# Optimization experiments

Measured on AMD Instinct MI355X. Metric: run time of the kernel, lower is better.

Reference implementation:

```python
import jax, jax.numpy as jnp
import numpy as np

VOCAB, S, D, H, DH, L, W1S, DFF = 50265, 4096, 768, 12, 64, 2, 256, 3072


def layer_norm(x, g, b, eps=1e-5):
    m = jnp.mean(x, axis=-1, keepdims=True)
    v = jnp.mean((x - m) ** 2, axis=-1, keepdims=True)
    return (x - m) * jax.lax.rsqrt(v + eps) * g + b


def sliding_global_attn(q, k, v, att, w=W1S):
    # q,k,v: [B,H,S,Dh]; att: [B,S] float (1 real / 0 pad). Longformer-style
    # sliding window (one-sided w) + global attention on token 0.
    B, nh, S_, Dh = q.shape
    nc = S_ // w
    q = q * (Dh ** -0.5)
    k_pad = jnp.pad(k, ((0, 0), (0, 0), (w, w), (0, 0)))
    v_pad = jnp.pad(v, ((0, 0), (0, 0), (w, w), (0, 0)))
    idx = jnp.arange(nc)[:, None] * w + jnp.arange(3 * w)[None, :]  # [nc,3w] into padded axis
    k_band = k_pad[:, :, idx]  # [B,H,nc,3w,Dh]
    v_band = v_pad[:, :, idx]
    qc = q.reshape(B, nh, nc, w, Dh)
    s_loc = jnp.einsum('bhcqd,bhckd->bhcqk', qc, k_band)  # [B,H,nc,w,3w]
    rel = jnp.arange(3 * w)[None, :] - jnp.arange(w)[:, None]  # [w,3w]
    band_ok = (rel >= 0) & (rel <= 2 * w)
    key_abs = idx - w  # [nc,3w] absolute key positions
    in_seq = (key_abs >= 0) & (key_abs < S_) & (key_abs != 0)  # token 0 handled by global column
    key_real = att[:, jnp.clip(key_abs, 0, S_ - 1)] > 0  # [B,nc,3w]
    valid = band_ok[None, None, None] & in_seq[None, None, :, None, :] & key_real[:, None, :, None, :]
    s_loc = jnp.where(valid, s_loc, -1e9)
    s_g = jnp.einsum('bhcqd,bhd->bhcq', qc, k[:, :, 0])  # global key column
    p = jax.nn.softmax(jnp.concatenate([s_g[..., None], s_loc], axis=-1), axis=-1)
    out = (jnp.einsum('bhcq,bhd->bhcqd', p[..., 0], v[:, :, 0])
           + jnp.einsum('bhcqk,bhckd->bhcqd', p[..., 1:], v_band)).reshape(B, nh, S_, Dh)
    # global token 0 attends to everything
    s0 = jnp.where(att[:, None, :] > 0, jnp.einsum('bhd,bhsd->bhs', q[:, :, 0], k), -1e9)
    out0 = jnp.einsum('bhs,bhsd->bhd', jax.nn.softmax(s0, axis=-1), v)
    return out.at[:, :, 0].set(out0)


def setup_inputs() -> dict:
    key = jax.random.key(0)
    ks = jax.random.split(key, 16)
    sc = 0.02
    inp = {
        'input_ids': jax.random.randint(ks[0], (2, S), 0, VOCAB, dtype=jnp.int64)
        if jax.config.jax_enable_x64 else jax.random.randint(ks[0], (2, S), 0, VOCAB, dtype=jnp.int32),
        'attention_mask': jnp.ones((2, S), dtype=jnp.int32),
        'word_emb': sc * jax.random.normal(ks[1], (VOCAB, D), jnp.float32),
        'pos_emb': sc * jax.random.normal(ks[2], (S, D), jnp.float32),
        'emb_ln_g': jnp.ones((D,), jnp.float32), 'emb_ln_b': jnp.zeros((D,), jnp.float32),
        'Wq': sc * jax.random.normal(ks[3], (L, D, D), jnp.float32), 'bq': jnp.zeros((L, D), jnp.float32),
        'Wk': sc * jax.random.normal(ks[4], (L, D, D), jnp.float32), 'bk': jnp.zeros((L, D), jnp.float32),
        'Wv': sc * jax.random.normal(ks[5], (L, D, D), jnp.float32), 'bv': jnp.zeros((L, D), jnp.float32),
        'Wo': sc * jax.random.normal(ks[6], (L, D, D), jnp.float32), 'bo': jnp.zeros((L, D), jnp.float32),
        'ln1_g': jnp.ones((L, D), jnp.float32), 'ln1_b': jnp.zeros((L, D), jnp.float32),
        'Wf1': sc * jax.random.normal(ks[7], (L, D, DFF), jnp.float32), 'bf1': jnp.zeros((L, DFF), jnp.float32),
        'Wf2': sc * jax.random.normal(ks[8], (L, DFF, D), jnp.float32), 'bf2': jnp.zeros((L, D), jnp.float32),
        'ln2_g': jnp.ones((L, D), jnp.float32), 'ln2_b': jnp.zeros((L, D), jnp.float32),
        'Wh1': sc * jax.random.normal(ks[9], (D, 256), jnp.float32), 'bh1': jnp.zeros((256,), jnp.float32),
        'Wh2': sc * jax.random.normal(ks[10], (256, 14), jnp.float32), 'bh2': jnp.zeros((14,), jnp.float32),
    }
    return inp


def reference(input_ids, attention_mask, word_emb, pos_emb, emb_ln_g, emb_ln_b,
              Wq, bq, Wk, bk, Wv, bv, Wo, bo, ln1_g, ln1_b,
              Wf1, bf1, Wf2, bf2, ln2_g, ln2_b, Wh1, bh1, Wh2, bh2):
    B, S_ = input_ids.shape
    att = attention_mask.astype(jnp.float32)
    x = word_emb[input_ids] + pos_emb[None, :S_, :]
    x = layer_norm(x, emb_ln_g, emb_ln_b)
    for l in range(L):
        def heads(w, b):
            return (x @ w + b).reshape(B, S_, H, DH).transpose(0, 2, 1, 3)
        q = heads(Wq[l], bq[l]); k = heads(Wk[l], bk[l]); v = heads(Wv[l], bv[l])
        a = sliding_global_attn(q, k, v, att)
        a = a.transpose(0, 2, 1, 3).reshape(B, S_, D) @ Wo[l] + bo[l]
        x = layer_norm(x + a, ln1_g[l], ln1_b[l])
        f = jax.nn.gelu(x @ Wf1[l] + bf1[l]) @ Wf2[l] + bf2[l]
        x = layer_norm(x + f, ln2_g[l], ln2_b[l])
    # masked mean pool
    m = att[..., None]
    pooled = jnp.sum(x * m, axis=1) / jnp.clip(jnp.sum(m, axis=1), 1e-9)
    h = jax.nn.relu(pooled @ Wh1 + bh1)
    return jax.nn.sigmoid(h @ Wh2 + bh2) * 4.0
```

## Files before the change

kernel.cpp:

```cpp
#include <hip/hip_runtime.h>
#include <hip/hip_bf16.h>
#include <math.h>

#define S_LEN 4096
#define D_MODEL 768
#define NHEAD 12
#define DH 64
#define NLAYER 2
#define DFF 3072
#define BATCH 2
#define QSTR 2304

typedef __attribute__((ext_vector_type(8))) __bf16 bf16x8;
typedef __attribute__((ext_vector_type(4))) float f32x4;
typedef __attribute__((ext_vector_type(16))) float f32x16;

__device__ __forceinline__ unsigned short f2bf_bits(float f) {
  unsigned int u = __float_as_uint(f);
  unsigned int r = (u + 0x7fffu + ((u >> 16) & 1u)) >> 16;
  return (unsigned short)r;
}

__device__ __forceinline__ float bf2f(unsigned short u) {
  return __uint_as_float(((unsigned int)u) << 16);
}

__device__ __forceinline__ unsigned int cvtpk_bf16(float lo, float hi) {
  unsigned int d;
  asm("v_cvt_pk_bf16_f32 %0, %1, %2" : "=v"(d) : "v"(lo), "v"(hi));
  return d;
}

__device__ __forceinline__ float gelu_fast(float x) {
  float u = 0.7978845608028654f * (x + 0.044715f * x * x * x);
  float t2 = fminf(fmaxf(2.f * u, -18.f), 18.f);
  float e = __expf(t2);
  return 0.5f * x * (1.f + (e - 1.f) / (e + 1.f));
}

#define ASYNC_COPY16(gsrc, ldst)                                       \
  __builtin_amdgcn_global_load_lds(                                    \
      (const __attribute__((address_space(1))) void*)(gsrc),           \
      (__attribute__((address_space(3))) void*)(ldst), 16, 0, 0)

#define MFMA_BF16(a, b, c) __builtin_amdgcn_mfma_f32_16x16x32_bf16(a, b, c, 0, 0, 0)
#define MFMA32_BF16(a, b, c) __builtin_amdgcn_mfma_f32_32x32x16_bf16(a, b, c, 0, 0, 0)

__device__ __forceinline__ float blk_sum256(float v, float* lds) {
#pragma unroll
  for (int off = 32; off > 0; off >>= 1) v += __shfl_down(v, off, 64);
  __syncthreads();
  if ((threadIdx.x & 63) == 0) lds[threadIdx.x >> 6] = v;
  __syncthreads();
  return lds[0] + lds[1] + lds[2] + lds[3];
}

__global__ __launch_bounds__(256) void wconv_kernel(
    const float* __restrict__ Wq, const float* __restrict__ Wk,
    const float* __restrict__ Wv, const float* __restrict__ Wo,
    const float* __restrict__ Wf1, const float* __restrict__ Wf2,
    unsigned short* __restrict__ Wbf) {
  int id = blockIdx.x;
  const float* src;
  unsigned short* dst;
  int K, N, t;
  if (id < 4608) {
    int m = id / 576;
    t = id % 576;
    int layer = m >> 2, which = m & 3;
    const float* s = (which == 0) ? Wq : (which == 1) ? Wk : (which == 2) ? Wv : Wo;
    src = s + (size_t)layer * 589824;
    dst = Wbf + (size_t)layer * 7077888 + (size_t)which * 589824;
    K = 768; N = 768;
  } else if (id < 9216) {
    int j = id - 4608;
    int layer = j / 2304;
    t = j % 2304;
    src = Wf1 + (size_t)layer * 2359296;
    dst = Wbf + (size_t)layer * 7077888 + 2359296;
    K = 768; N = 3072;
  } else {
    int j = id - 9216;
    int layer = j / 2304;
    t = j % 2304;
    src = Wf2 + (size_t)layer * 2359296;
    dst = Wbf + (size_t)layer * 7077888 + 4718592;
    K = 3072; N = 768;
  }
  int tiles_n = N >> 5;
  int tk = t / tiles_n, tn = t % tiles_n;
  __shared__ float tile[32][33];
  int c = threadIdx.x & 31, r0 = threadIdx.x >> 5;
#pragma unroll
  for (int p = 0; p < 4; ++p) {
    int r = r0 + p * 8;
    tile[r][c] = src[(size_t)(tk * 32 + r) * N + tn * 32 + c];
  }
  __syncthreads();
#pragma unroll
  for (int p = 0; p < 4; ++p) {
    int r = r0 + p * 8;
    dst[(size_t)(tn * 32 + r) * K + tk * 32 + c] = f2bf_bits(tile[c][r]);
  }
}

__global__ __launch_bounds__(256) void mask_kernel(
    const int* __restrict__ att, float* __restrict__ maskF) {
  int i = blockIdx.x * 256 + threadIdx.x;
  int b = i >> 12, ka = i & 4095;
  maskF[i] = (ka >= 1 && att[b * S_LEN + ka] > 0) ? 0.f : -1e9f;
}

__global__ __launch_bounds__(256) void embed_ln_kernel(
    const int* __restrict__ ids, const float* __restrict__ wemb,
    const float* __restrict__ pemb, const float* __restrict__ g,
    const float* __restrict__ b, unsigned short* __restrict__ Xb) {
  int row = blockIdx.x;
  int s = row % S_LEN;
  int id = ids[row];
  const float* we = wemb + (size_t)id * D_MODEL;
  const float* pe = pemb + (size_t)s * D_MODEL;
  int t = threadIdx.x;
  __shared__ float lds[4];
  float v0 = we[t] + pe[t];
  float v1 = we[t + 256] + pe[t + 256];
  float v2 = we[t + 512] + pe[t + 512];
  float mean = blk_sum256(v0 + v1 + v2, lds) * (1.f / 768.f);
  float d0 = v0 - mean, d1 = v1 - mean, d2 = v2 - mean;
  float var = blk_sum256(d0 * d0 + d1 * d1 + d2 * d2, lds) * (1.f / 768.f);
  float rs = rsqrtf(var + 1e-5f);
  unsigned short* xb = Xb + (size_t)row * D_MODEL;
  xb[t]       = f2bf_bits(d0 * rs * g[t] + b[t]);
  xb[t + 256] = f2bf_bits(d1 * rs * g[t + 256] + b[t + 256]);
  xb[t + 512] = f2bf_bits(d2 * rs * g[t + 512] + b[t + 512]);
}

__global__ __launch_bounds__(256) void ln_kernel(
    const float* __restrict__ T, const float* __restrict__ g,
    const float* __restrict__ b, unsigned short* __restrict__ Xb) {
  int row = blockIdx.x;
  const float* tp = T + (size_t)row * D_MODEL;
  int t = threadIdx.x;
  __shared__ float lds[4];
  float v0 = tp[t], v1 = tp[t + 256], v2 = tp[t + 512];
  float mean = blk_sum256(v0 + v1 + v2, lds) * (1.f / 768.f);
  float d0 = v0 - mean, d1 = v1 - mean, d2 = v2 - mean;
  float var = blk_sum256(d0 * d0 + d1 * d1 + d2 * d2, lds) * (1.f / 768.f);
  float rs = rsqrtf(var + 1e-5f);
  unsigned short* xb = Xb + (size_t)row * D_MODEL;
  xb[t]       = f2bf_bits(d0 * rs * g[t] + b[t]);
  xb[t + 256] = f2bf_bits(d1 * rs * g[t + 256] + b[t + 256]);
  xb[t + 512] = f2bf_bits(d2 * rs * g[t + 512] + b[t + 512]);
}

template <int MODE>
__global__ __launch_bounds__(256) void gemm32(
    const unsigned short* __restrict__ A, const unsigned short* __restrict__ Bt,
    const float* __restrict__ bias0, const float* __restrict__ bias1,
    const float* __restrict__ bias2, const unsigned short* __restrict__ ResBf,
    void* __restrict__ Cout, int M, int N, int K) {
  __shared__ unsigned short Abuf[3][128 * 32];
  __shared__ unsigned short Bbuf[3][128 * 32];
  const int tid = threadIdx.x;
  const int lane = tid & 63, w = tid >> 6;
  const int wm = w >> 1, wn = w & 1;
  const int l31 = lane & 31, l5 = lane >> 5;

  const int nbx = gridDim.x;
  const int nwg = nbx * gridDim.y;
  const int orig = blockIdx.y * nbx + blockIdx.x;
  const int wgid = (orig & 7) * (nwg >> 3) + (orig >> 3);
  const int m0 = (wgid / nbx) * 128, n0 = (wgid % nbx) * 128;

  f32x16 acc[2][2];
#pragma unroll
  for (int i = 0; i < 2; ++i)
#pragma unroll
    for (int j = 0; j < 2; ++j)
#pragma unroll
      for (int r = 0; r < 16; ++r) acc[i][j][r] = 0.f;

  const int s0 = w * 64 + lane, s1 = s0 + 256;
  const int r0 = s0 >> 2, c0 = (s0 & 3) ^ ((r0 >> 1) & 3);
  const int r1 = s1 >> 2, c1 = (s1 & 3) ^ ((r1 >> 1) & 3);
  const unsigned short* gA0 = A + (size_t)(m0 + r0) * K + c0 * 8;
  const unsigned short* gA1 = A + (size_t)(m0 + r1) * K + c1 * 8;
  const unsigned short* gB0 = Bt + (size_t)(n0 + r0) * K + c0 * 8;
  const unsigned short* gB1 = Bt + (size_t)(n0 + r1) * K + c1 * 8;
  const int dA0 = (w * 64) * 8, dA1 = (256 + w * 64) * 8;

  int aoff[2][2], boff[2][2];
#pragma unroll
  for (int mt = 0; mt < 2; ++mt) {
    int ra = wm * 64 + mt * 32 + l31;
    int rb = wn * 64 + mt * 32 + l31;
    int key_a = (ra >> 1) & 3, key_b = (rb >> 1) & 3;
#pragma unroll
    for (int ks = 0; ks < 2; ++ks) {
      aoff[mt][ks] = ra * 32 + ((((ks << 1) | l5) ^ key_a) << 3);
      boff[mt][ks] = rb * 32 + ((((ks << 1) | l5) ^ key_b) << 3);
    }
  }

#define STAGE(bsel)                                                       \
  {                                                                       \
    ASYNC_COPY16(gA0, &Abuf[bsel][dA0]);                                  \
    ASYNC_COPY16(gA1, &Abuf[bsel][dA1]);                                  \
    ASYNC_COPY16(gB0, &Bbuf[bsel][dA0]);                                  \
    ASYNC_COPY16(gB1, &Bbuf[bsel][dA1]);                                  \
    gA0 += 32; gA1 += 32; gB0 += 32; gB1 += 32;                           \
  }

  const int nk = K >> 5;
  STAGE(0);
  if (nk > 1) STAGE(1);
  asm volatile("s_waitcnt vmcnt(4)" ::: "memory");
  __builtin_amdgcn_s_barrier();
  __builtin_amdgcn_sched_barrier(0);

  int cur = 0;
  for (int kt = 0; kt < nk; ++kt) {
    if (kt + 2 < nk) {
      int nxt = cur + 2;
      if (nxt >= 3) nxt -= 3;
      STAGE(nxt);
    }
    bf16x8 av[2][2], bv[2][2];
#pragma unroll
    for (int mt = 0; mt < 2; ++mt)
#pragma unroll
      for (int ks = 0; ks < 2; ++ks) {
        av[mt][ks] = *(const bf16x8*)(&Abuf[cur][aoff[mt][ks]]);
        bv[mt][ks] = *(const bf16x8*)(&Bbuf[cur][boff[mt][ks]]);
      }
#pragma unroll
    for (int mt = 0; mt < 2; ++mt)
#pragma unroll
      for (int nt = 0; nt < 2; ++nt)
#pragma unroll
        for (int ks = 0; ks < 2; ++ks)
          acc[mt][nt] = MFMA32_BF16(av[mt][ks], bv[nt][ks], acc[mt][nt]);
    if (kt + 1 < nk) {
      if (kt + 2 < nk)
        asm volatile("s_waitcnt vmcnt(4)" ::: "memory");
      else
        asm volatile("s_waitcnt vmcnt(0)" ::: "memory");
      __builtin_amdgcn_s_barrier();
      __builtin_amdgcn_sched_barrier(0);
    }
    cur = (cur == 2) ? 0 : cur + 1;
  }
#undef STAGE

#pragma unroll
  for (int mt = 0; mt < 2; ++mt) {
#pragma unroll
    for (int nt = 0; nt < 2; ++nt) {
      int gc = n0 + wn * 64 + nt * 32 + l31;
      float bsv;
      if (MODE == 4)
        bsv = (gc < 768) ? bias0[gc] : (gc < 1536) ? bias1[gc - 768] : bias2[gc - 1536];
      else
        bsv = bias0[gc];
#pragma unroll
      for (int reg = 0; reg < 16; ++reg) {
        int gr = m0 + wm * 64 + mt * 32 + (reg & 3) + 8 * (reg >> 2) + 4 * l5;
        float v = acc[mt][nt][reg] + bsv;
        if (MODE == 1) v = gelu_fast(v);
        if (MODE == 4 && gc < 768) v *= 0.125f;
        if (MODE == 2) {
          v += bf2f(ResBf[(size_t)gr * 768 + gc]);
          ((float*)Cout)[(size_t)gr * N + gc] = v;
        } else {
          ((unsigned short*)Cout)[(size_t)gr * N + gc] = f2bf_bits(v);
        }
      }
    }
  }
}

__global__ __launch_bounds__(256) void vtrans_kernel(
    const unsigned short* __restrict__ Vsrc, unsigned short* __restrict__ Vt) {
  int kb = blockIdx.x, h = blockIdx.y, b = blockIdx.z;
  int k0 = kb * 64;
  const size_t bs = (size_t)b * S_LEN;
  const size_t bh = (size_t)(b * NHEAD + h);
  __shared__ unsigned short tile[64][72];
  int tid = threadIdx.x;
#pragma unroll
  for (int p = 0; p < 2; ++p) {
    int idx = p * 256 + tid;
    int key = idx >> 3, ch = idx & 7;
    bf16x8 v = *(const bf16x8*)(Vsrc + (bs + k0 + key) * QSTR + h * DH + ch * 8);
    *(bf16x8*)&tile[key][ch * 8] = v;
  }
  __syncthreads();
#pragma unroll
  for (int p = 0; p < 2; ++p) {
    int idx = p * 256 + tid;
    int d = idx >> 3, kc = idx & 7;
    unsigned int w0 = tile[kc * 8 + 0][d] | ((unsigned int)tile[kc * 8 + 1][d] << 16);
    unsigned int w1 = tile[kc * 8 + 2][d] | ((unsigned int)tile[kc * 8 + 3][d] << 16);
    unsigned int w2 = tile[kc * 8 + 4][d] | ((unsigned int)tile[kc * 8 + 5][d] << 16);
    unsigned int w3 = tile[kc * 8 + 6][d] | ((unsigned int)tile[kc * 8 + 7][d] << 16);
    uint4 out = make_uint4(w0, w1, w2, w3);
    *(uint4*)(Vt + (bh * 64 + d) * S_LEN + k0 + kc * 8) = out;
  }
}

__global__ __launch_bounds__(512) void band_attn_kernel(
    const unsigned short* __restrict__ Qg, const unsigned short* __restrict__ Kgb,
    const unsigned short* __restrict__ Vgb, const unsigned short* __restrict__ Vt,
    const int* __restrict__ att, const float* __restrict__ maskF,
    unsigned short* __restrict__ Aout) {
  const int bid = blockIdx.x;
  const int tid = threadIdx.x;
  const int lane = tid & 63, wq = tid >> 6;
  const int g = lane >> 4, cl = lane & 15;

  __shared__ __align__(16) float smemg[4680];

  if (bid >= 384) {
    int g2 = bid - 384;
    int h = g2 % NHEAD, b = g2 / NHEAD;
    const size_t bs = (size_t)b * S_LEN;
    float* sc = smemg;
    float* q0 = sc + S_LEN;
    float* red = q0 + 64;
    float* part = red + 8;
    if (tid < 64) q0[tid] = bf2f(Qg[bs * QSTR + h * DH + tid]);
    __syncthreads();
    float lmax = -1e30f;
    for (int s = tid; s < S_LEN; s += 512) {
      const unsigned short* kp = Kgb + (bs + s) * QSTR + h * DH;
      float acc = 0.f;
#pragma unroll
      for (int cc = 0; cc < 8; ++cc) {
        uint4 u = *(const uint4*)(kp + cc * 8);
        const unsigned int* uu = (const unsigned int*)&u;
#pragma unroll
        for (int w2 = 0; w2 < 4; ++w2) {
          unsigned int x = uu[w2];
          acc += q0[cc * 8 + w2 * 2] * __uint_as_float(x << 16);
          acc += q0[cc * 8 + w2 * 2 + 1] * __uint_as_float(x & 0xffff0000u);
        }
      }
      acc = (att[b * S_LEN + s] > 0) ? acc : -1e9f;
      sc[s] = acc;
      lmax = fmaxf(lmax, acc);
    }
#pragma unroll
    for (int off = 32; off > 0; off >>= 1) lmax = fmaxf(lmax, __shfl_down(lmax, off, 64));
    __syncthreads();
    if (lane == 0) red[wq] = lmax;
    __syncthreads();
    float M = red[0];
#pragma unroll
    for (int i = 1; i < 8; ++i) M = fmaxf(M, red[i]);
    float lsum = 0.f;
    for (int s = tid; s < S_LEN; s += 512) {
      float p = __expf(sc[s] - M);
      sc[s] = p;
      lsum += p;
    }
#pragma unroll
    for (int off = 32; off > 0; off >>= 1) lsum += __shfl_down(lsum, off, 64);
    __syncthreads();
    if (lane == 0) red[wq] = lsum;
    __syncthreads();
    float L = red[0];
#pragma unroll
    for (int i = 1; i < 8; ++i) L += red[i];
    int d = tid & 63, chunk = tid >> 6;
    float acc2 = 0.f;
    for (int s = chunk * 512; s < (chunk + 1) * 512; ++s)
      acc2 += sc[s] * bf2f(Vgb[(bs + s) * QSTR + h * DH + d]);
    part[chunk * 64 + d] = acc2;
    __syncthreads();
    if (tid < 64) {
      float v = 0.f;
#pragma unroll
      for (int i = 0; i < 8; ++i) v += part[i * 64 + tid];
      Aout[bs * D_MODEL + h * DH + tid] = f2bf_bits(v / L);
    }
    return;
  }

  const int xcd = bid & 7, within = bid >> 3;
  const int flat = xcd * 48 + within;
  const int c = flat & 15;
  const int hb = flat >> 4;
  const int h = hb % NHEAD, b = hb / NHEAD;
  const size_t bs = (size_t)b * S_LEN;
  const size_t bh = (size_t)(b * NHEAD + h);
  const int Q0 = c * 256;

  bf16x8 qf[2][2];
#pragma unroll
  for (int qt = 0; qt < 2; ++qt)
#pragma unroll
    for (int ks = 0; ks < 2; ++ks)
      qf[qt][ks] = *(const bf16x8*)(Qg + (bs + Q0 + wq * 32 + qt * 16 + cl) * QSTR +
                                    h * DH + ks * 32 + g * 8);

  float mrun[2], lrun[2];
  f32x4 oacc[2][4];
#pragma unroll
  for (int qt = 0; qt < 2; ++qt) {
    float sg = 0.f;
#pragma unroll
    for (int ks = 0; ks < 2; ++ks) {
      bf16x8 k0 = *(const bf16x8*)(Kgb + bs * QSTR + h * DH + ks * 32 + g * 8);
#pragma unroll
      for (int j = 0; j < 8; ++j) sg += (float)qf[qt][ks][j] * (float)k0[j];
    }
    sg += __shfl_xor(sg, 16, 64);
    sg += __shfl_xor(sg, 32, 64);
    mrun[qt] = sg;
    lrun[qt] = 1.f;
  }
#pragma unroll
  for (int dt = 0; dt < 4; ++dt) {
    float v0d = bf2f(Vgb[bs * QSTR + h * DH + dt * 16 + cl]);
    f32x4 vv = {v0d, v0d, v0d, v0d};
    oacc[0][dt] = vv;
    oacc[1][dt] = vv;
  }

  const int jlo = wq * 32, jhi = wq * 32 + 543;
  const int tlo = (Q0 < 256) ? 4 : 0;
  int thi = (S_LEN + 256 - Q0) >> 6;
  if (thi > 12) thi = 12;

  for (int t = tlo; t < thi; ++t) {
    if (t * 64 + 63 < jlo || t * 64 > jhi) continue;
    const int kabs0 = Q0 - 256 + t * 64;

    f32x4 accs[4][2];
#pragma unroll
    for (int kt = 0; kt < 4; ++kt) {
      accs[kt][0] = (f32x4){0.f, 0.f, 0.f, 0.f};
      accs[kt][1] = (f32x4){0.f, 0.f, 0.f, 0.f};
    }
#pragma unroll
    for (int ks = 0; ks < 2; ++ks) {
      bf16x8 kf[4];
#pragma unroll
      for (int kt = 0; kt < 4; ++kt)
        kf[kt] = *(const bf16x8*)(Kgb + (bs + kabs0 + kt * 16 + cl) * QSTR +
                                  h * DH + ks * 32 + g * 8);
#pragma unroll
      for (int kt = 0; kt < 4; ++kt) {
        accs[kt][0] = MFMA_BF16(kf[kt], qf[0][ks], accs[kt][0]);
        accs[kt][1] = MFMA_BF16(kf[kt], qf[1][ks], accs[kt][1]);
      }
    }

    float4 mk[4];
#pragma unroll
    for (int kt = 0; kt < 4; ++kt)
      mk[kt] = *(const float4*)(maskF + b * S_LEN + kabs0 + kt * 16 + g * 4);

#pragma unroll
    for (int qt = 0; qt < 2; ++qt) {
      int iq = wq * 32 + qt * 16 + cl;
      int relbase = t * 64 - iq;
      float pvv[4][4];
      float tmax = -1e30f;
#pragma unroll
      for (int kt = 0; kt < 4; ++kt) {
        const float* mkf = (const float*)&mk[kt];
#pragma unroll
        for (int r = 0; r < 4; ++r) {
          int key = kt * 16 + g * 4 + r;
          int rel = relbase + key;
          float x = accs[kt][qt][r] + mkf[r];
          x = (rel >= 0 && rel <= 512) ? x : -1e9f;
          pvv[kt][r] = x;
          tmax = fmaxf(tmax, x);
        }
      }
      tmax = fmaxf(tmax, __shfl_xor(tmax, 16, 64));
      tmax = fmaxf(tmax, __shfl_xor(tmax, 32, 64));
      float mnew = fmaxf(mrun[qt], tmax);
      float scale = __expf(mrun[qt] - mnew);
      mrun[qt] = mnew;
      float psum = 0.f;
#pragma unroll
      for (int kt = 0; kt < 4; ++kt)
#pragma unroll
        for (int r = 0; r < 4; ++r) {
          float pp = __expf(pvv[kt][r] - mnew);
          pvv[kt][r] = pp;
          psum += pp;
        }
      psum += __shfl_xor(psum, 16, 64);
      psum += __shfl_xor(psum, 32, 64);
      lrun[qt] = lrun[qt] * scale + psum;
      float scr[4];
#pragma unroll
      for (int r = 0; r < 4; ++r) scr[r] = __shfl(scale, g * 4 + r, 64);
#pragma unroll
      for (int dt = 0; dt < 4; ++dt) {
        oacc[qt][dt][0] *= scr[0];
        oacc[qt][dt][1] *= scr[1];
        oacc[qt][dt][2] *= scr[2];
        oacc[qt][dt][3] *= scr[3];
      }
#pragma unroll
      for (int ks = 0; ks < 2; ++ks) {
        unsigned int E0D0 = cvtpk_bf16(pvv[ks * 2][0], pvv[ks * 2][1]);
        unsigned int E0D1 = cvtpk_bf16(pvv[ks * 2][2], pvv[ks * 2][3]);
        unsigned int E1D0 = cvtpk_bf16(pvv[ks * 2 + 1][0], pvv[ks * 2 + 1][1]);
        unsigned int E1D1 = cvtpk_bf16(pvv[ks * 2 + 1][2], pvv[ks * 2 + 1][3]);
        int src0 = ((lane >> 4) & 1) * 32 + cl;
        int src1 = src0 + 16;
        unsigned int a0 = (unsigned int)__shfl((int)E0D0, src0, 64);
        unsigned int a1 = (unsigned int)__shfl((int)E0D1, src0, 64);
        unsigned int a2 = (unsigned int)__shfl((int)E0D0, src1, 64);
        unsigned int a3 = (unsigned int)__shfl((int)E0D1, src1, 64);
        unsigned int b0 = (unsigned int)__shfl((int)E1D0, src0, 64);
        unsigned int b1 = (unsigned int)__shfl((int)E1D1, src0, 64);
        unsigned int b2 = (unsigned int)__shfl((int)E1D0, src1, 64);
        unsigned int b3 = (unsigned int)__shfl((int)E1D1, src1, 64);
        bool hi = lane >= 32;
        union { unsigned int u[4]; bf16x8 v; } af;
        af.u[0] = hi ? b0 : a0;
        af.u[1] = hi ? b1 : a1;
        af.u[2] = hi ? b2 : a2;
        af.u[3] = hi ? b3 : a3;
#pragma unroll
        for (int dt = 0; dt < 4; ++dt) {
          bf16x8 vf = *(const bf16x8*)(Vt + (bh * 64 + dt * 16 + cl) * S_LEN +
                                       kabs0 + (ks * 4 + g) * 8);
          oacc[qt][dt] = MFMA_BF16(af.v, vf, oacc[qt][dt]);
        }
      }
    }
  }

#pragma unroll
  for (int qt = 0; qt < 2; ++qt) {
    float lr[4];
#pragma unroll
    for (int r = 0; r < 4; ++r) lr[r] = 1.f / __shfl(lrun[qt], g * 4 + r, 64);
#pragma unroll
    for (int dt = 0; dt < 4; ++dt)
#pragma unroll
      for (int r = 0; r < 4; ++r) {
        int row = Q0 + wq * 32 + qt * 16 + g * 4 + r;
        if (row != 0)
          Aout[(bs + row) * D_MODEL + h * DH + dt * 16 + cl] =
              f2bf_bits(oacc[qt][dt][r] * lr[r]);
      }
  }
}

__global__ __launch_bounds__(256) void pool1_kernel(
    const unsigned short* __restrict__ Xb, const int* __restrict__ att,
    float* __restrict__ ppart) {
  int sb = blockIdx.x, b = blockIdx.y, t = threadIdx.x;
  float a0 = 0.f, a1 = 0.f, a2 = 0.f;
  for (int s = sb * 256; s < sb * 256 + 256; ++s) {
    float a = (float)att[b * S_LEN + s];
    const unsigned short* xp = Xb + ((size_t)b * S_LEN + s) * D_MODEL;
    a0 += bf2f(xp[t]) * a; a1 += bf2f(xp[t + 256]) * a; a2 += bf2f(xp[t + 512]) * a;
  }
  float* pp = ppart + ((size_t)b * 16 + sb) * D_MODEL;
  pp[t] = a0; pp[t + 256] = a1; pp[t + 512] = a2;
}

__global__ __launch_bounds__(256) void pool2_kernel(
    const float* __restrict__ ppart, const int* __restrict__ att,
    float* __restrict__ pooled) {
  int b = blockIdx.x, t = threadIdx.x;
  float a0 = 0.f, a1 = 0.f, a2 = 0.f;
  for (int sb = 0; sb < 16; ++sb) {
    const float* pp = ppart + ((size_t)b * 16 + sb) * D_MODEL;
    a0 += pp[t]; a1 += pp[t + 256]; a2 += pp[t + 512];
  }
  float cnt = 0.f;
  for (int s = 0; s < S_LEN; ++s) cnt += (float)att[b * S_LEN + s];
  cnt = fmaxf(cnt, 1e-9f);
  pooled[b * D_MODEL + t]       = a0 / cnt;
  pooled[b * D_MODEL + t + 256] = a1 / cnt;
  pooled[b * D_MODEL + t + 512] = a2 / cnt;
}

__global__ __launch_bounds__(256) void head_kernel(
    const float* __restrict__ pooled, const float* __restrict__ Wh1,
    const float* __restrict__ bh1, const float* __restrict__ Wh2,
    const float* __restrict__ bh2, float* __restrict__ out) {
  __shared__ float hbuf[2][256];
  int t = threadIdx.x;
  for (int b = 0; b < 2; ++b) {
    float acc = bh1[t];
    for (int d = 0; d < D_MODEL; ++d) acc += pooled[b * D_MODEL + d] * Wh1[d * 256 + t];
    hbuf[b][t] = fmaxf(acc, 0.f);
  }
  __syncthreads();
  if (t < 28) {
    int b = t / 14, j = t % 14;
    float acc = bh2[j];
    for (int i = 0; i < 256; ++i) acc += hbuf[b][i] * Wh2[i * 14 + j];
    out[t] = 4.f / (1.f + __expf(-acc));
  }
}

extern "C" void kernel_launch(void* const* d_in, const int* in_sizes, int n_in,
                              void* d_out, int out_size, void* d_ws,
                              size_t ws_size, hipStream_t stream) {
  const int* ids    = (const int*)d_in[0];
  const int* att    = (const int*)d_in[1];
  const float* wemb = (const float*)d_in[2];
  const float* pemb = (const float*)d_in[3];
  const float* elng = (const float*)d_in[4];
  const float* elnb = (const float*)d_in[5];
  const float* Wq   = (const float*)d_in[6];
  const float* bq   = (const float*)d_in[7];
  const float* Wk   = (const float*)d_in[8];
  const float* bk   = (const float*)d_in[9];
  const float* Wv   = (const float*)d_in[10];
  const float* bv   = (const float*)d_in[11];
  const float* Wo   = (const float*)d_in[12];
  const float* bo   = (const float*)d_in[13];
  const float* ln1g = (const float*)d_in[14];
  const float* ln1b = (const float*)d_in[15];
  const float* Wf1  = (const float*)d_in[16];
  const float* bf1  = (const float*)d_in[17];
  const float* Wf2  = (const float*)d_in[18];
  const float* bf2  = (const float*)d_in[19];
  const float* ln2g = (const float*)d_in[20];
  const float* ln2b = (const float*)d_in[21];
  const float* Wh1  = (const float*)d_in[22];
  const float* bh1  = (const float*)d_in[23];
  const float* Wh2  = (const float*)d_in[24];
  const float* bh2  = (const float*)d_in[25];

  const int M = BATCH * S_LEN;
  float* ws = (float*)d_ws;
  float* T = ws;
  unsigned short* QKV  = (unsigned short*)(ws + 6291456);
  unsigned short* Vt   = (unsigned short*)(ws + 11010048);
  unsigned short* Abbf = (unsigned short*)(ws + 12582912);
  unsigned short* Xbf  = (unsigned short*)(ws + 15728640);
  unsigned short* FFbf = (unsigned short*)(ws + 18874368);
  unsigned short* Wbf  = (unsigned short*)(ws + 31457280);
  float* pooled = ws + 38535168;
  float* ppart  = ws + 38536704;
  float* maskF  = ws + 38561280;

  wconv_kernel<<<13824, 256, 0, stream>>>(Wq, Wk, Wv, Wo, Wf1, Wf2, Wbf);
  mask_kernel<<<32, 256, 0, stream>>>(att, maskF);
  embed_ln_kernel<<<M, 256, 0, stream>>>(ids, wemb, pemb, elng, elnb, Xbf);

  for (int l = 0; l < NLAYER; ++l) {
    const unsigned short* wqkv = Wbf + (size_t)l * 7077888;
    const unsigned short* wot  = wqkv + 1769472;
    const unsigned short* wf1t = wqkv + 2359296;
    const unsigned short* wf2t = wqkv + 4718592;

    gemm32<4><<<dim3(18, 64), 256, 0, stream>>>(
        Xbf, wqkv, bq + l * D_MODEL, bk + l * D_MODEL, bv + l * D_MODEL,
        nullptr, QKV, M, QSTR, 768);

    vtrans_kernel<<<dim3(64, NHEAD, BATCH), 256, 0, stream>>>(QKV + 1536, Vt);
    band_attn_kernel<<<408, 512, 0, stream>>>(
        QKV, QKV + 768, QKV + 1536, Vt, att, maskF, Abbf);

    gemm32<2><<<dim3(6, 64), 256, 0, stream>>>(
        Abbf, wot, bo + l * D_MODEL, nullptr, nullptr, Xbf, T, M, 768, 768);
    ln_kernel<<<M, 256, 0, stream>>>(T, ln1g + l * D_MODEL, ln1b + l * D_MODEL, Xbf);

    gemm32<1><<<dim3(24, 64), 256, 0, stream>>>(
        Xbf, wf1t, bf1 + l * DFF, nullptr, nullptr, nullptr, FFbf, M, DFF, 768);
    gemm32<2><<<dim3(6, 64), 256, 0, stream>>>(
        FFbf, wf2t, bf2 + l * D_MODEL, nullptr, nullptr, Xbf, T, M, 768, DFF);
    ln_kernel<<<M, 256, 0, stream>>>(T, ln2g + l * D_MODEL, ln2b + l * D_MODEL, Xbf);
  }

  pool1_kernel<<<dim3(16, BATCH), 256, 0, stream>>>(Xbf, att, ppart);
  pool2_kernel<<<BATCH, 256, 0, stream>>>(ppart, att, pooled);
  head_kernel<<<1, 256, 0, stream>>>(pooled, Wh1, bh1, Wh2, bh2, (float*)d_out);
}
```

Before: 851.1 us.

## Rewrite band attention with 32x32 MFMA, per-wave key range, smaller blocks

The band attention kernel moves from 16x16x16 MFMA tiles with two query subtiles per wave to 32x32 MFMA tiles, where each lane owns one query row and the softmax reductions need only a single cross-half shuffle. Each wave now loops only over the key tiles its own 32 queries touch, replacing the fixed 12-tile loop that skipped tiles with a branch. Blocks shrink to 256 threads and 128 queries, doubling the grid, and the global-token path is adjusted to four waves. The aim is fewer shuffles, less wasted tile work and better occupancy and load balance. The P-operand lane shuffling for the second MFMA is new and error-prone.

```diff
diff --git a/kernel.cpp b/kernel.cpp
--- a/kernel.cpp
+++ b/kernel.cpp
@@ -308,7 +308,7 @@
   }
 }
 
-__global__ __launch_bounds__(512) void band_attn_kernel(
+__global__ __launch_bounds__(256) void band_attn_kernel(
     const unsigned short* __restrict__ Qg, const unsigned short* __restrict__ Kgb,
     const unsigned short* __restrict__ Vgb, const unsigned short* __restrict__ Vt,
     const int* __restrict__ att, const float* __restrict__ maskF,
@@ -316,12 +316,12 @@
   const int bid = blockIdx.x;
   const int tid = threadIdx.x;
   const int lane = tid & 63, wq = tid >> 6;
-  const int g = lane >> 4, cl = lane & 15;
-
-  __shared__ __align__(16) float smemg[4680];
-
-  if (bid >= 384) {
-    int g2 = bid - 384;
+  const int l31 = lane & 31, l5 = lane >> 5;
+
+  __shared__ __align__(16) float smemg[4424];
+
+  if (bid >= 768) {
+    int g2 = bid - 768;
     int h = g2 % NHEAD, b = g2 / NHEAD;
     const size_t bs = (size_t)b * S_LEN;
     float* sc = smemg;
@@ -331,7 +331,7 @@
     if (tid < 64) q0[tid] = bf2f(Qg[bs * QSTR + h * DH + tid]);
     __syncthreads();
     float lmax = -1e30f;
-    for (int s = tid; s < S_LEN; s += 512) {
+    for (int s = tid; s < S_LEN; s += 256) {
       const unsigned short* kp = Kgb + (bs + s) * QSTR + h * DH;
       float acc = 0.f;
 #pragma unroll
@@ -354,11 +354,9 @@
     __syncthreads();
     if (lane == 0) red[wq] = lmax;
     __syncthreads();
-    float M = red[0];
-#pragma unroll
-    for (int i = 1; i < 8; ++i) M = fmaxf(M, red[i]);
+    float M = fmaxf(fmaxf(red[0], red[1]), fmaxf(red[2], red[3]));
     float lsum = 0.f;
-    for (int s = tid; s < S_LEN; s += 512) {
+    for (int s = tid; s < S_LEN; s += 256) {
       float p = __expf(sc[s] - M);
       sc[s] = p;
       lsum += p;
@@ -368,190 +366,161 @@
     __syncthreads();
     if (lane == 0) red[wq] = lsum;
     __syncthreads();
-    float L = red[0];
-#pragma unroll
-    for (int i = 1; i < 8; ++i) L += red[i];
+    float L = red[0] + red[1] + red[2] + red[3];
     int d = tid & 63, chunk = tid >> 6;
     float acc2 = 0.f;
-    for (int s = chunk * 512; s < (chunk + 1) * 512; ++s)
+    for (int s = chunk * 1024; s < (chunk + 1) * 1024; ++s)
       acc2 += sc[s] * bf2f(Vgb[(bs + s) * QSTR + h * DH + d]);
     part[chunk * 64 + d] = acc2;
     __syncthreads();
     if (tid < 64) {
-      float v = 0.f;
-#pragma unroll
-      for (int i = 0; i < 8; ++i) v += part[i * 64 + tid];
+      float v = part[tid] + part[64 + tid] + part[128 + tid] + part[192 + tid];
       Aout[bs * D_MODEL + h * DH + tid] = f2bf_bits(v / L);
     }
     return;
   }
 
   const int xcd = bid & 7, within = bid >> 3;
-  const int flat = xcd * 48 + within;
-  const int c = flat & 15;
-  const int hb = flat >> 4;
+  const int flat = xcd * 96 + within;
+  const int c = flat & 31;
+  const int hb = flat >> 5;
   const int h = hb % NHEAD, b = hb / NHEAD;
   const size_t bs = (size_t)b * S_LEN;
   const size_t bh = (size_t)(b * NHEAD + h);
-  const int Q0 = c * 256;
-
-  bf16x8 qf[2][2];
-#pragma unroll
-  for (int qt = 0; qt < 2; ++qt)
-#pragma unroll
-    for (int ks = 0; ks < 2; ++ks)
-      qf[qt][ks] = *(const bf16x8*)(Qg + (bs + Q0 + wq * 32 + qt * 16 + cl) * QSTR +
-                                    h * DH + ks * 32 + g * 8);
-
-  float mrun[2], lrun[2];
-  f32x4 oacc[2][4];
-#pragma unroll
-  for (int qt = 0; qt < 2; ++qt) {
+  const int qbase = c * 128 + wq * 32;
+  const int iq = qbase + l31;
+
+  bf16x8 qfr[4];
+#pragma unroll
+  for (int ks = 0; ks < 4; ++ks)
+    qfr[ks] = *(const bf16x8*)(Qg + (bs + iq) * QSTR + h * DH + ks * 16 + l5 * 8);
+
+  float mrun, lrun;
+  {
     float sg = 0.f;
 #pragma unroll
-    for (int ks = 0; ks < 2; ++ks) {
-      bf16x8 k0 = *(const bf16x8*)(Kgb + bs * QSTR + h * DH + ks * 32 + g * 8);
-#pragma unroll
-      for (int j = 0; j < 8; ++j) sg += (float)qf[qt][ks][j] * (float)k0[j];
-    }
-    sg += __shfl_xor(sg, 16, 64);
+    for (int ks = 0; ks < 4; ++ks) {
+      bf16x8 k0 = *(const bf16x8*)(Kgb + bs * QSTR + h * DH + ks * 16 + l5 * 8);
+#pragma unroll
+      for (int j = 0; j < 8; ++j) sg += (float)qfr[ks][j] * (float)k0[j];
+    }
     sg += __shfl_xor(sg, 32, 64);
-    mrun[qt] = sg;
-    lrun[qt] = 1.f;
-  }
-#pragma unroll
-  for (int dt = 0; dt < 4; ++dt) {
-    float v0d = bf2f(Vgb[bs * QSTR + h * DH + dt * 16 + cl]);
-    f32x4 vv = {v0d, v0d, v0d, v0d};
-    oacc[0][dt] = vv;
-    oacc[1][dt] = vv;
-  }
-
-  const int jlo = wq * 32, jhi = wq * 32 + 543;
-  const int tlo = (Q0 < 256) ? 4 : 0;
-  int thi = (S_LEN + 256 - Q0) >> 6;
-  if (thi > 12) thi = 12;
-
-  for (int t = tlo; t < thi; ++t) {
-    if (t * 64 + 63 < jlo || t * 64 > jhi) continue;
-    const int kabs0 = Q0 - 256 + t * 64;
-
-    f32x4 accs[4][2];
-#pragma unroll
-    for (int kt = 0; kt < 4; ++kt) {
-      accs[kt][0] = (f32x4){0.f, 0.f, 0.f, 0.f};
-      accs[kt][1] = (f32x4){0.f, 0.f, 0.f, 0.f};
-    }
-#pragma unroll
-    for (int ks = 0; ks < 2; ++ks) {
-      bf16x8 kf[4];
-#pragma unroll
-      for (int kt = 0; kt < 4; ++kt)
-        kf[kt] = *(const bf16x8*)(Kgb + (bs + kabs0 + kt * 16 + cl) * QSTR +
-                                  h * DH + ks * 32 + g * 8);
-#pragma unroll
-      for (int kt = 0; kt < 4; ++kt) {
-        accs[kt][0] = MFMA_BF16(kf[kt], qf[0][ks], accs[kt][0]);
-        accs[kt][1] = MFMA_BF16(kf[kt], qf[1][ks], accs[kt][1]);
-      }
-    }
-
-    float4 mk[4];
-#pragma unroll
-    for (int kt = 0; kt < 4; ++kt)
-      mk[kt] = *(const float4*)(maskF + b * S_LEN + kabs0 + kt * 16 + g * 4);
-
-#pragma unroll
-    for (int qt = 0; qt < 2; ++qt) {
-      int iq = wq * 32 + qt * 16 + cl;
-      int relbase = t * 64 - iq;
-      float pvv[4][4];
-      float tmax = -1e30f;
-#pragma unroll
-      for (int kt = 0; kt < 4; ++kt) {
-        const float* mkf = (const float*)&mk[kt];
-#pragma unroll
-        for (int r = 0; r < 4; ++r) {
-          int key = kt * 16 + g * 4 + r;
-          int rel = relbase + key;
-          float x = accs[kt][qt][r] + mkf[r];
+    mrun = sg;
+    lrun = 1.f;
+  }
+
+  f32x16 oacc[2];
+#pragma unroll
+  for (int ds = 0; ds < 2; ++ds)
+#pragma unroll
+    for (int qd = 0; qd < 4; ++qd) {
+      int d0 = ds * 32 + 8 * qd + 4 * l5;
+      uint2 u = *(const uint2*)(Vgb + bs * QSTR + h * DH + d0);
+      oacc[ds][qd * 4 + 0] = bf2f((unsigned short)(u.x & 0xffffu));
+      oacc[ds][qd * 4 + 1] = bf2f((unsigned short)(u.x >> 16));
+      oacc[ds][qd * 4 + 2] = bf2f((unsigned short)(u.y & 0xffffu));
+      oacc[ds][qd * 4 + 3] = bf2f((unsigned short)(u.y >> 16));
+    }
+
+  const int ka0 = (qbase >> 6) << 6;
+  int lastk = qbase + 543;
+  if (lastk > S_LEN - 1) lastk = S_LEN - 1;
+  const int nt = ((lastk - ka0) >> 6) + 1;
+
+  for (int ti = 0; ti < nt; ++ti) {
+    const int kabs0 = ka0 + ti * 64;
+
+    f32x16 sacc[2];
+#pragma unroll
+    for (int r = 0; r < 16; ++r) { sacc[0][r] = 0.f; sacc[1][r] = 0.f; }
+#pragma unroll
+    for (int ks = 0; ks < 4; ++ks) {
+      bf16x8 kf0 = *(const bf16x8*)(Kgb + (bs + kabs0 + l31) * QSTR + h * DH + ks * 16 + l5 * 8);
+      bf16x8 kf1 = *(const bf16x8*)(Kgb + (bs + kabs0 + 32 + l31) * QSTR + h * DH + ks * 16 + l5 * 8);
+      sacc[0] = MFMA32_BF16(kf0, qfr[ks], sacc[0]);
+      sacc[1] = MFMA32_BF16(kf1, qfr[ks], sacc[1]);
+    }
+
+    float tmax = -1e30f;
+#pragma unroll
+    for (int s = 0; s < 2; ++s) {
+#pragma unroll
+      for (int mg = 0; mg < 4; ++mg) {
+        float4 mk = *(const float4*)(maskF + b * S_LEN + kabs0 + s * 32 + 8 * mg + 4 * l5);
+        const float* mkf = (const float*)&mk;
+#pragma unroll
+        for (int e = 0; e < 4; ++e) {
+          int off = s * 32 + 8 * mg + 4 * l5 + e;
+          int rel = kabs0 + off - iq;
+          float x = sacc[s][mg * 4 + e] + mkf[e];
           x = (rel >= 0 && rel <= 512) ? x : -1e9f;
-          pvv[kt][r] = x;
+          sacc[s][mg * 4 + e] = x;
           tmax = fmaxf(tmax, x);
         }
       }
-      tmax = fmaxf(tmax, __shfl_xor(tmax, 16, 64));
-      tmax = fmaxf(tmax, __shfl_xor(tmax, 32, 64));
-      float mnew = fmaxf(mrun[qt], tmax);
-      float scale = __expf(mrun[qt] - mnew);
-      mrun[qt] = mnew;
-      float psum = 0.f;
-#pragma unroll
-      for (int kt = 0; kt < 4; ++kt)
-#pragma unroll
-        for (int r = 0; r < 4; ++r) {
-          float pp = __expf(pvv[kt][r] - mnew);
-          pvv[kt][r] = pp;
-          psum += pp;
+    }
+    tmax = fmaxf(tmax, __shfl_xor(tmax, 32, 64));
+    float mnew = fmaxf(mrun, tmax);
+    float scale = __expf(mrun - mnew);
+    mrun = mnew;
+    float psum = 0.f;
+#pragma unroll
+    for (int s = 0; s < 2; ++s)
+#pragma unroll
+      for (int r = 0; r < 16; ++r) {
+        float p = __expf(sacc[s][r] - mnew);
+        sacc[s][r] = p;
+        psum += p;
+      }
+    psum += __shfl_xor(psum, 32, 64);
+    lrun = lrun * scale + psum;
+#pragma unroll
+    for (int ds = 0; ds < 2; ++ds)
+#pragma unroll
+      for (int r = 0; r < 16; ++r) oacc[ds][r] *= scale;
+
+    unsigned own[2][4][2], part[2][4][2];
+#pragma unroll
+    for (int s = 0; s < 2; ++s)
+#pragma unroll
+      for (int mg = 0; mg < 4; ++mg)
+#pragma unroll
+        for (int p = 0; p < 2; ++p) {
+          own[s][mg][p] = cvtpk_bf16(sacc[s][4 * mg + 2 * p], sacc[s][4 * mg + 2 * p + 1]);
+          part[s][mg][p] = (unsigned)__shfl_xor((int)own[s][mg][p], 32, 64);
         }
-      psum += __shfl_xor(psum, 16, 64);
-      psum += __shfl_xor(psum, 32, 64);
-      lrun[qt] = lrun[qt] * scale + psum;
-      float scr[4];
-#pragma unroll
-      for (int r = 0; r < 4; ++r) scr[r] = __shfl(scale, g * 4 + r, 64);
-#pragma unroll
-      for (int dt = 0; dt < 4; ++dt) {
-        oacc[qt][dt][0] *= scr[0];
-        oacc[qt][dt][1] *= scr[1];
-        oacc[qt][dt][2] *= scr[2];
-        oacc[qt][dt][3] *= scr[3];
+
+#pragma unroll
+    for (int cc = 0; cc < 4; ++cc) {
+      const int s = cc >> 1, hh = cc & 1;
+      unsigned moA0 = l5 ? own[s][2 * hh + 1][0] : own[s][2 * hh][0];
+      unsigned moA1 = l5 ? own[s][2 * hh + 1][1] : own[s][2 * hh][1];
+      unsigned mpA0 = l5 ? part[s][2 * hh + 1][0] : part[s][2 * hh][0];
+      unsigned mpA1 = l5 ? part[s][2 * hh + 1][1] : part[s][2 * hh][1];
+      union { unsigned u[4]; bf16x8 v; } bfr;
+      bfr.u[0] = l5 ? mpA0 : moA0;
+      bfr.u[1] = l5 ? mpA1 : moA1;
+      bfr.u[2] = l5 ? moA0 : mpA0;
+      bfr.u[3] = l5 ? moA1 : mpA1;
+#pragma unroll
+      for (int ds = 0; ds < 2; ++ds) {
+        bf16x8 av = *(const bf16x8*)(Vt + (bh * 64 + ds * 32 + l31) * S_LEN +
+                                     kabs0 + cc * 16 + l5 * 8);
+        oacc[ds] = MFMA32_BF16(av, bfr.v, oacc[ds]);
       }
-#pragma unroll
-      for (int ks = 0; ks < 2; ++ks) {
-        unsigned int E0D0 = cvtpk_bf16(pvv[ks * 2][0], pvv[ks * 2][1]);
-        unsigned int E0D1 = cvtpk_bf16(pvv[ks * 2][2], pvv[ks * 2][3]);
-        unsigned int E1D0 = cvtpk_bf16(pvv[ks * 2 + 1][0], pvv[ks * 2 + 1][1]);
-        unsigned int E1D1 = cvtpk_bf16(pvv[ks * 2 + 1][2], pvv[ks * 2 + 1][3]);
-        int src0 = ((lane >> 4) & 1) * 32 + cl;
-        int src1 = src0 + 16;
-        unsigned int a0 = (unsigned int)__shfl((int)E0D0, src0, 64);
-        unsigned int a1 = (unsigned int)__shfl((int)E0D1, src0, 64);
-        unsigned int a2 = (unsigned int)__shfl((int)E0D0, src1, 64);
-        unsigned int a3 = (unsigned int)__shfl((int)E0D1, src1, 64);
-        unsigned int b0 = (unsigned int)__shfl((int)E1D0, src0, 64);
-        unsigned int b1 = (unsigned int)__shfl((int)E1D1, src0, 64);
-        unsigned int b2 = (unsigned int)__shfl((int)E1D0, src1, 64);
-        unsigned int b3 = (unsigned int)__shfl((int)E1D1, src1, 64);
-        bool hi = lane >= 32;
-        union { unsigned int u[4]; bf16x8 v; } af;
-        af.u[0] = hi ? b0 : a0;
-        af.u[1] = hi ? b1 : a1;
-        af.u[2] = hi ? b2 : a2;
-        af.u[3] = hi ? b3 : a3;
-#pragma unroll
-        for (int dt = 0; dt < 4; ++dt) {
-          bf16x8 vf = *(const bf16x8*)(Vt + (bh * 64 + dt * 16 + cl) * S_LEN +
-                                       kabs0 + (ks * 4 + g) * 8);
-          oacc[qt][dt] = MFMA_BF16(af.v, vf, oacc[qt][dt]);
-        }
-      }
-    }
-  }
-
-#pragma unroll
-  for (int qt = 0; qt < 2; ++qt) {
-    float lr[4];
-#pragma unroll
-    for (int r = 0; r < 4; ++r) lr[r] = 1.f / __shfl(lrun[qt], g * 4 + r, 64);
-#pragma unroll
-    for (int dt = 0; dt < 4; ++dt)
-#pragma unroll
-      for (int r = 0; r < 4; ++r) {
-        int row = Q0 + wq * 32 + qt * 16 + g * 4 + r;
-        if (row != 0)
-          Aout[(bs + row) * D_MODEL + h * DH + dt * 16 + cl] =
-              f2bf_bits(oacc[qt][dt][r] * lr[r]);
+    }
+  }
+
+  float inv = 1.f / lrun;
+  if (iq != 0) {
+#pragma unroll
+    for (int ds = 0; ds < 2; ++ds)
+#pragma unroll
+      for (int qd = 0; qd < 4; ++qd) {
+        int d0 = ds * 32 + 8 * qd + 4 * l5;
+        unsigned lo = cvtpk_bf16(oacc[ds][qd * 4 + 0] * inv, oacc[ds][qd * 4 + 1] * inv);
+        unsigned hi = cvtpk_bf16(oacc[ds][qd * 4 + 2] * inv, oacc[ds][qd * 4 + 3] * inv);
+        *(uint2*)(Aout + (bs + iq) * D_MODEL + h * DH + d0) = make_uint2(lo, hi);
       }
   }
 }
@@ -665,7 +634,7 @@
         nullptr, QKV, M, QSTR, 768);
 
     vtrans_kernel<<<dim3(64, NHEAD, BATCH), 256, 0, stream>>>(QKV + 1536, Vt);
-    band_attn_kernel<<<408, 512, 0, stream>>>(
+    band_attn_kernel<<<792, 256, 0, stream>>>(
         QKV, QKV + 768, QKV + 1536, Vt, att, maskF, Abbf);
 
     gemm32<2><<<dim3(6, 64), 256, 0, stream>>>(
```

After: 947.3 us. 1.11x slower.
